# Performance work log

Hardware: AMD Instinct MI355X
Metric: run time of the kernel (lower is better)

Reference implementation:

```python
import jax, jax.numpy as jnp
import numpy as np
from jax import lax

IN_DIM, HID_DIM, OUT_DIM = 1024, 2048, 1024
N_EXP_A, TOPK_A, N_EXP_G = 12, 4, 6
BATCH = 2048
# Shannon entropy (nats) of {1/2, 1/3, 1/6}
H_TARGET = float(-(0.5 * np.log(0.5) + (1.0 / 3.0) * np.log(1.0 / 3.0) + (1.0 / 6.0) * np.log(1.0 / 6.0)))


def setup_inputs() -> dict:
    key = jax.random.key(0)
    ks = jax.random.split(key, 24)
    s_in = 1.0 / np.sqrt(IN_DIM)
    s_hid = 1.0 / np.sqrt(HID_DIM)
    s_out = 1.0 / np.sqrt(OUT_DIM)
    d = {}
    d['x'] = jax.random.normal(ks[0], (BATCH, IN_DIM), dtype=jnp.float32)
    # EngineA: gate + 12 experts (stacked)
    d['gate_a_w'] = jax.random.normal(ks[1], (IN_DIM, N_EXP_A), jnp.float32) * s_in
    d['gate_a_b'] = jnp.zeros((N_EXP_A,), jnp.float32)
    d['wa1'] = jax.random.normal(ks[2], (N_EXP_A, IN_DIM, HID_DIM), jnp.float32) * s_in
    d['ba1'] = jnp.zeros((N_EXP_A, HID_DIM), jnp.float32)
    d['wa2'] = jax.random.normal(ks[3], (N_EXP_A, HID_DIM, OUT_DIM), jnp.float32) * s_hid
    d['ba2'] = jnp.zeros((N_EXP_A, OUT_DIM), jnp.float32)
    # EngineG: gate + 6 experts (stacked)
    d['gate_g_w'] = jax.random.normal(ks[4], (IN_DIM, N_EXP_G), jnp.float32) * s_in
    d['gate_g_b'] = jnp.zeros((N_EXP_G,), jnp.float32)
    d['wg1'] = jax.random.normal(ks[5], (N_EXP_G, IN_DIM, HID_DIM), jnp.float32) * s_in
    d['bg1'] = jnp.zeros((N_EXP_G, HID_DIM), jnp.float32)
    d['wg2'] = jax.random.normal(ks[6], (N_EXP_G, HID_DIM, OUT_DIM), jnp.float32) * s_hid
    d['bg2'] = jnp.zeros((N_EXP_G, OUT_DIM), jnp.float32)
    # self_model: Linear(3,hid) Tanh Linear(hid,out) Tanh
    d['sm_w1'] = jax.random.normal(ks[7], (3, HID_DIM), jnp.float32) * (1.0 / np.sqrt(3.0))
    d['sm_b1'] = jnp.zeros((HID_DIM,), jnp.float32)
    d['sm_w2'] = jax.random.normal(ks[8], (HID_DIM, OUT_DIM), jnp.float32) * s_hid
    d['sm_b2'] = jnp.zeros((OUT_DIM,), jnp.float32)
    # self_influence Linear(out,out)
    d['si_w'] = jax.random.normal(ks[9], (OUT_DIM, OUT_DIM), jnp.float32) * s_out
    d['si_b'] = jnp.zeros((OUT_DIM,), jnp.float32)
    # field_transform Linear(out,out) + Tanh
    d['ft_w'] = jax.random.normal(ks[10], (OUT_DIM, OUT_DIM), jnp.float32) * s_out
    d['ft_b'] = jnp.zeros((OUT_DIM,), jnp.float32)
    d['tension_scale'] = jnp.asarray(1.0 / 3.0, jnp.float32)
    d['n_steps'] = 3
    return d


def _experts(x, w1, b1, w2, b2):
    # x:[B,I], w1:[E,I,H] -> [B,E,O]  (Linear-ReLU-Linear per expert)
    h = jax.nn.relu(jnp.einsum('bi,eih->beh', x, w1) + b1[None])
    return jnp.einsum('beh,eho->beo', h, w2) + b2[None]


def reference(x, gate_a_w, gate_a_b, wa1, ba1, wa2, ba2,
              gate_g_w, gate_g_b, wg1, bg1, wg2, bg2,
              sm_w1, sm_b1, sm_w2, sm_b2, si_w, si_b, ft_w, ft_b,
              tension_scale, n_steps):
    B = x.shape[0]
    # ---- EngineA: top-k (k=4 of 12) MoE ----
    logits_a = x @ gate_a_w + gate_a_b
    topv, topi = lax.top_k(logits_a, TOPK_A)
    topw = jax.nn.softmax(topv, axis=-1)
    weights_a = jnp.zeros_like(logits_a).at[jnp.arange(B)[:, None], topi].set(topw)
    out_a = _experts(x, wa1, ba1, wa2, ba2)            # [B,12,O]
    out_plus = jnp.einsum('be,beo->bo', weights_a, out_a)
    # ---- EngineG: dense-softmax MoE + entropy loss ----
    weights_g = jax.nn.softmax(x @ gate_g_w + gate_g_b, axis=-1)
    out_g = _experts(x, wg1, bg1, wg2, bg2)            # [B,6,O]
    out_minus = jnp.einsum('be,beo->bo', weights_g, out_g)
    h_ent = -(weights_g * jnp.log(weights_g + 1e-8)).sum(-1).mean()
    entropy_loss = (h_ent - H_TARGET) ** 2
    # ---- self-referential loop ----
    repulsion = out_plus - out_minus
    prev_tension = (repulsion ** 2).sum(-1, keepdims=True)      # [B,1]
    tensions = [lax.stop_gradient(prev_tension.mean())]          # .item() detaches
    modified_repulsion = repulsion
    for step in range(n_steps):
        tension_scalar = prev_tension.mean(-1, keepdims=True)    # [B,1]
        if step == 0:
            tension_delta = jnp.zeros_like(tension_scalar)
        else:
            tension_delta = tension_scalar - tensions[-1]
        step_tensor = jnp.full_like(tension_scalar, step / n_steps)
        self_input = jnp.concatenate([tension_scalar, tension_delta, step_tensor], -1)  # [B,3]
        self_state = jnp.tanh(jnp.tanh(self_input @ sm_w1 + sm_b1) @ sm_w2 + sm_b2)
        influence = self_state @ si_w + si_b
        modified_repulsion = repulsion + influence
        prev_tension = (modified_repulsion ** 2).sum(-1, keepdims=True)
        tensions.append(lax.stop_gradient(prev_tension.mean()))
    equilibrium = (out_plus + out_minus) * 0.5
    field_direction = jnp.tanh(modified_repulsion @ ft_w + ft_b)
    output = equilibrium + tension_scale * jnp.sqrt(prev_tension + 1e-8) * field_direction
    t = jnp.stack(tensions)
    convergence_loss = jnp.abs(t[1:] - t[:-1]).mean()            # built from .item()s -> constant
    aux_loss = entropy_loss + 0.001 * convergence_loss
    return output, aux_loss
```

## Files before the change

kernel.cpp:

```cpp
#include <hip/hip_runtime.h>

typedef _Float16 f16;
typedef f16  f16x8 __attribute__((ext_vector_type(8)));
typedef f16  f16x4 __attribute__((ext_vector_type(4)));
typedef float f32x4 __attribute__((ext_vector_type(4)));

#define LOAD_LDS16(gp, lp) __builtin_amdgcn_global_load_lds( \
    (const __attribute__((address_space(1))) void*)(gp),     \
    (__attribute__((address_space(3))) void*)(lp), 16, 0, 0)


__global__ __launch_bounds__(256) void castx_kernel(const float* __restrict__ x,
                                                    f16* __restrict__ o) {
  long i = ((long)blockIdx.x * 256 + threadIdx.x) * 4;
  const float4 v = *(const float4*)(x + i);
  f16x4 h; h.x = (f16)v.x; h.y = (f16)v.y; h.z = (f16)v.z; h.w = (f16)v.w;
  *(f16x4*)(o + i) = h;
}

__global__ __launch_bounds__(256) void transpose_cast(const float* __restrict__ src,
                                                      f16* __restrict__ dst,
                                                      int R, int C, long sbatch,
                                                      long dbatch, int dld) {
  __shared__ float tile[32][33];
  const int zc = blockIdx.x * 32;
  const int zr = blockIdx.y * 32;
  const int z  = blockIdx.z;
  const float* s = src + (long)z * sbatch;
  f16* d = dst + (long)z * dbatch;
  const int tx = threadIdx.x & 31, ty = threadIdx.x >> 5;
#pragma unroll
  for (int rr = 0; rr < 32; rr += 8)
    tile[ty + rr][tx] = s[(long)(zr + ty + rr) * C + (zc + tx)];
  __syncthreads();
#pragma unroll
  for (int rr = 0; rr < 32; rr += 8)
    d[(long)(zc + ty + rr) * dld + (zr + tx)] = (f16)tile[tx][ty + rr];
}

__global__ __launch_bounds__(256) void gating_kernel(
    const float* __restrict__ x, const float* __restrict__ gaw,
    const float* __restrict__ gab, const float* __restrict__ ggw,
    const float* __restrict__ ggb,
    float* __restrict__ wG, float* __restrict__ ent,
    int* __restrict__ rows, float* __restrict__ gval, int* __restrict__ cnt,
    int* __restrict__ eA, int* __restrict__ posA, float* __restrict__ wA4) {
  const int b = blockIdx.x, t = threadIdx.x;
  const float* xr = x + (long)b * 1024;
  float pa[12], pg[6];
#pragma unroll
  for (int e = 0; e < 12; e++) pa[e] = 0.f;
#pragma unroll
  for (int e = 0; e < 6; e++) pg[e] = 0.f;
  const int i0 = t * 4;
  const float4 xv = *(const float4*)(xr + i0);
  const float xs[4] = {xv.x, xv.y, xv.z, xv.w};
#pragma unroll
  for (int u = 0; u < 4; u++) {
    const float xi = xs[u];
    const float* ga = gaw + (long)(i0 + u) * 12;
    const float* gg = ggw + (long)(i0 + u) * 6;
#pragma unroll
    for (int e = 0; e < 12; e++) pa[e] += xi * ga[e];
#pragma unroll
    for (int e = 0; e < 6; e++) pg[e] += xi * gg[e];
  }
#pragma unroll
  for (int e = 0; e < 12; e++)
    for (int m = 1; m < 64; m <<= 1) pa[e] += __shfl_xor(pa[e], m);
#pragma unroll
  for (int e = 0; e < 6; e++)
    for (int m = 1; m < 64; m <<= 1) pg[e] += __shfl_xor(pg[e], m);
  __shared__ float rw[4][18];
  const int lane = t & 63, wv = t >> 6;
  if (lane == 0) {
#pragma unroll
    for (int e = 0; e < 12; e++) rw[wv][e] = pa[e];
#pragma unroll
    for (int e = 0; e < 6; e++) rw[wv][12 + e] = pg[e];
  }
  __syncthreads();
  if (t == 0) {
    float la[12], lg[6];
#pragma unroll
    for (int e = 0; e < 12; e++)
      la[e] = rw[0][e] + rw[1][e] + rw[2][e] + rw[3][e] + gab[e];
#pragma unroll
    for (int e = 0; e < 6; e++)
      lg[e] = rw[0][12 + e] + rw[1][12 + e] + rw[2][12 + e] + rw[3][12 + e] + ggb[e];
    unsigned used = 0; float tv[4]; int tix[4];
    for (int k = 0; k < 4; k++) {
      float best = -3.4e38f; int bi = 0;
      for (int e = 0; e < 12; e++)
        if (!((used >> e) & 1u) && la[e] > best) { best = la[e]; bi = e; }
      tv[k] = best; tix[k] = bi; used |= 1u << bi;
    }
    const float mx = tv[0];
    float s = 0.f, w4[4];
    for (int k = 0; k < 4; k++) { w4[k] = expf(tv[k] - mx); s += w4[k]; }
    for (int k = 0; k < 4; k++) {
      const float w = w4[k] / s;
      const int e = tix[k];
      const int pos = atomicAdd(&cnt[e], 1);
      rows[e * 2048 + pos] = b;
      gval[e * 2048 + pos] = w;
      eA[b * 4 + k] = e;
      posA[b * 4 + k] = pos;
      wA4[b * 4 + k] = w;
    }
    float mg = lg[0];
    for (int e = 1; e < 6; e++) mg = fmaxf(mg, lg[e]);
    float sg = 0.f, wg6[6];
    for (int e = 0; e < 6; e++) { wg6[e] = expf(lg[e] - mg); sg += wg6[e]; }
    float H = 0.f;
    for (int e = 0; e < 6; e++) {
      const float w = wg6[e] / sg;
      wG[b * 6 + e] = w;
      H -= w * logf(w + 1e-8f);
    }
    ent[b] = H;
  }
}

__global__ void base_kernel(const int* __restrict__ cnt, int* __restrict__ baseA) {
  if (threadIdx.x == 0 && blockIdx.x == 0) {
    int r = 0;
    for (int e = 0; e < 12; e++) { baseA[e] = r; r += cnt[e]; }
  }
}

__global__ __launch_bounds__(256) void combine_kernel(
    const f16* __restrict__ res, const int* __restrict__ eA,
    const int* __restrict__ posA, const float* __restrict__ wA4,
    const float* __restrict__ wG, const int* __restrict__ baseA,
    const float* __restrict__ ba2, const float* __restrict__ bg2,
    float* __restrict__ outP, float* __restrict__ outM,
    float* __restrict__ pt0, float* __restrict__ ts0) {
  const long b = blockIdx.x;
  const int t = threadIdx.x;
  const int c = t * 4;
  float4 P = {0.f, 0.f, 0.f, 0.f}, M = {0.f, 0.f, 0.f, 0.f};
#pragma unroll
  for (int k = 0; k < 4; k++) {
    const int e = eA[b * 4 + k];
    const long slot = baseA[e] + posA[b * 4 + k];
    const f16x4 v = *(const f16x4*)(res + slot * 1024 + c);
    const float w = wA4[b * 4 + k];
    const float4 bb = *(const float4*)(ba2 + (long)e * 1024 + c);
    P.x += (float)v.x + w * bb.x; P.y += (float)v.y + w * bb.y;
    P.z += (float)v.z + w * bb.z; P.w += (float)v.w + w * bb.w;
  }
#pragma unroll
  for (int e = 0; e < 6; e++) {
    const f16x4 v = *(const f16x4*)(res + (8192L + e * 2048 + b) * 1024 + c);
    const float w = wG[b * 6 + e];
    const float4 bb = *(const float4*)(bg2 + (long)e * 1024 + c);
    M.x += (float)v.x + w * bb.x; M.y += (float)v.y + w * bb.y;
    M.z += (float)v.z + w * bb.z; M.w += (float)v.w + w * bb.w;
  }
  *(float4*)(outP + b * 1024 + c) = P;
  *(float4*)(outM + b * 1024 + c) = M;
  const float dx = P.x - M.x, dy = P.y - M.y, dz = P.z - M.z, dw = P.w - M.w;
  float s = dx * dx + dy * dy + dz * dz + dw * dw;
#pragma unroll
  for (int m = 1; m < 64; m <<= 1) s += __shfl_xor(s, m);
  __shared__ float rw[4];
  if ((t & 63) == 0) rw[t >> 6] = s;
  __syncthreads();
  if (t == 0) {
    const float tot = rw[0] + rw[1] + rw[2] + rw[3];
    pt0[b] = tot;
    atomicAdd(ts0, tot);
  }
}

__global__ __launch_bounds__(256) void hsm_kernel(
    const float* __restrict__ pt, const float* __restrict__ tsum,
    const float* __restrict__ w1, const float* __restrict__ b1,
    f16* __restrict__ o, int step) {
  const int j = blockIdx.x * 256 + threadIdx.x;
  const int b0 = blockIdx.y * 64;
  const float u0 = w1[j], u1 = w1[2048 + j], u2 = w1[4096 + j], bb = b1[j];
  const float tm = tsum[0] * (1.f / 2048.f);
  const float st = (float)step * (1.f / 3.f);
#pragma unroll 4
  for (int r = 0; r < 64; r++) {
    const int b = b0 + r;
    const float t = pt[b];
    const float delta = (step == 0) ? 0.f : (t - tm);
    o[(long)b * 2048 + j] = (f16)tanhf(t * u0 + delta * u1 + st * u2 + bb);
  }
}

__global__ __launch_bounds__(256) void aux_kernel(const float* __restrict__ ent,
                                                  const float* __restrict__ tsum,
                                                  float* __restrict__ out) {
  const int t = threadIdx.x;
  float s = 0.f;
  for (int i = t; i < 2048; i += 256) s += ent[i];
#pragma unroll
  for (int m = 1; m < 64; m <<= 1) s += __shfl_xor(s, m);
  __shared__ float rw[4];
  if ((t & 63) == 0) rw[t >> 6] = s;
  __syncthreads();
  if (t == 0) {
    const float h = (rw[0] + rw[1] + rw[2] + rw[3]) * (1.f / 2048.f);
    const float d = h - 1.0114042647f;
    const float el = d * d;
    const float t0 = tsum[0] * (1.f / 2048.f), t1 = tsum[1] * (1.f / 2048.f);
    const float t2 = tsum[2] * (1.f / 2048.f), t3 = tsum[3] * (1.f / 2048.f);
    const float conv = (fabsf(t1 - t0) + fabsf(t2 - t1) + fabsf(t3 - t2)) * (1.f / 3.f);
    out[0] = el + 0.001f * conv;
  }
}

__global__ __launch_bounds__(256) void gemm1_kernel(
    const f16* __restrict__ x, const f16* __restrict__ w1t,
    const float* __restrict__ ba1, const float* __restrict__ bg1,
    f16* __restrict__ h, const int* __restrict__ rows,
    const float* __restrict__ gval, const int* __restrict__ cnt,
    const int* __restrict__ baseA, const float* __restrict__ wG) {
  __shared__ f16 Al[2][128 * 32];
  __shared__ f16 Bl[2][128 * 32];
  __shared__ int   Lrow[128];
  __shared__ float Lg[128];
  int id = blockIdx.x;
  int e18, mi, ni, live; long row0; const float* bp;
  if (id < 3072) {
    const int k = id & 7, t = id >> 3;
    mi = t & 15; const int pid = k * 24 + (t >> 4);
    const int e = pid >> 4; ni = pid & 15;
    live = cnt[e] - mi * 128;
    if (live <= 0) return;
    if (live > 128) live = 128;
    row0 = baseA[e] + mi * 128; e18 = e; bp = ba1 + (long)e * 2048;
  } else {
    id -= 3072;
    const int k = id & 7, t = id >> 3;
    mi = t & 15; const int pid = k * 12 + (t >> 4);
    const int e = pid >> 4; ni = pid & 15;
    row0 = 8192L + e * 2048 + mi * 128; live = 128;
    e18 = 12 + e; bp = bg1 + (long)e * 2048;
  }
  const int tid = threadIdx.x;
  const bool routed = (e18 < 12);
  if (tid < 128) {
    const int gi = mi * 128 + tid;
    if (routed) {
      const bool ok = tid < live;
      Lrow[tid] = ok ? rows[e18 * 2048 + gi] : 0;
      Lg[tid]   = ok ? gval[e18 * 2048 + gi] : 0.f;
    } else {
      Lrow[tid] = gi;
      Lg[tid] = wG[gi * 6 + (e18 - 12)];
    }
  }
  __syncthreads();
  const int r0 = Lrow[tid >> 2], r1 = Lrow[64 + (tid >> 2)];
  const f16* a0 = x + (long)r0 * 1024 + (tid & 3) * 8;
  const f16* a1 = x + (long)r1 * 1024 + (tid & 3) * 8;
  const f16* b0 = w1t + (long)e18 * 2048 * 1024 + ((long)ni * 128 + (tid >> 2)) * 1024 + (tid & 3) * 8;
  const f16* b1p = b0 + 64 * 1024;

  const int wave = tid >> 6, lane = tid & 63;
  const int wm = wave & 1, wn = wave >> 1;
  const int l16 = lane & 15, q = lane >> 4;
  f32x4 acc[4][4] = {};

  LOAD_LDS16(a0, &Al[0][tid * 8]);
  LOAD_LDS16(a1, &Al[0][(256 + tid) * 8]);
  LOAD_LDS16(b0, &Bl[0][tid * 8]);
  LOAD_LDS16(b1p, &Bl[0][(256 + tid) * 8]);
  for (int kk = 0; kk < 32; ++kk) {
    __syncthreads();
    const int cur = kk & 1;
    if (kk + 1 < 32) {
      const long k0 = (long)(kk + 1) * 32;
      const int nb = cur ^ 1;
      LOAD_LDS16(a0 + k0, &Al[nb][tid * 8]);
      LOAD_LDS16(a1 + k0, &Al[nb][(256 + tid) * 8]);
      LOAD_LDS16(b0 + k0, &Bl[nb][tid * 8]);
      LOAD_LDS16(b1p + k0, &Bl[nb][(256 + tid) * 8]);
    }
    f16x8 av[4], bv[4];
#pragma unroll
    for (int i = 0; i < 4; i++)
      av[i] = *(const f16x8*)&Al[cur][(wm * 64 + i * 16 + l16) * 32 + q * 8];
#pragma unroll
    for (int j = 0; j < 4; j++)
      bv[j] = *(const f16x8*)&Bl[cur][(wn * 64 + j * 16 + l16) * 32 + q * 8];
#pragma unroll
    for (int i = 0; i < 4; i++)
#pragma unroll
      for (int j = 0; j < 4; j++)
        acc[i][j] = __builtin_amdgcn_mfma_f32_16x16x32_f16(av[i], bv[j], acc[i][j], 0, 0, 0);
  }
#pragma unroll
  for (int i = 0; i < 4; i++) {
#pragma unroll
    for (int r = 0; r < 4; r++) {
      const int lr = wm * 64 + i * 16 + q * 4 + r;
      if (lr < live) {
        const float wv = Lg[lr];
        f16* C = h + (row0 + lr) * 2048;
#pragma unroll
        for (int j = 0; j < 4; j++) {
          const int gc = ni * 128 + wn * 64 + j * 16 + l16;
          const float v = fmaxf(acc[i][j][r] + bp[gc], 0.f) * wv;
          C[gc] = (f16)v;
        }
      }
    }
  }
}

__global__ __launch_bounds__(256) void gemm2_kernel(
    const f16* __restrict__ h, const f16* __restrict__ w2t,
    f16* __restrict__ res, const int* __restrict__ cnt,
    const int* __restrict__ baseA) {
  __shared__ f16 Al[2][128 * 32];
  __shared__ f16 Bl[2][64 * 32];
  int id = blockIdx.x;
  int e18, mi, ni, live; long row0;
  if (id < 3072) {
    const int k = id & 7, t = id >> 3;
    mi = t & 15; const int pid = k * 24 + (t >> 4);
    const int e = pid >> 4; ni = pid & 15;
    live = cnt[e] - mi * 128;
    if (live <= 0) return;
    if (live > 128) live = 128;
    row0 = baseA[e] + mi * 128; e18 = e;
  } else {
    id -= 3072;
    const int k = id & 7, t = id >> 3;
    mi = t & 15; const int pid = k * 12 + (t >> 4);
    const int e = pid >> 4; ni = pid & 15;
    row0 = 8192L + e * 2048 + mi * 128; live = 128; e18 = 12 + e;
  }
  const int tid = threadIdx.x;
  const f16* a0 = h + (row0 + (tid >> 2)) * 2048 + (tid & 3) * 8;
  const f16* a1 = a0 + 64 * 2048;
  const f16* b0 = w2t + (long)e18 * 1024 * 2048 + ((long)ni * 64 + (tid >> 2)) * 2048 + (tid & 3) * 8;

  const int wave = tid >> 6, lane = tid & 63;
  const int wm = wave & 1, wn = wave >> 1;
  const int l16 = lane & 15, q = lane >> 4;
  f32x4 acc[4][2] = {};

  LOAD_LDS16(a0, &Al[0][tid * 8]);
  LOAD_LDS16(a1, &Al[0][(256 + tid) * 8]);
  LOAD_LDS16(b0, &Bl[0][tid * 8]);
  for (int kk = 0; kk < 64; ++kk) {
    __syncthreads();
    const int cur = kk & 1;
    if (kk + 1 < 64) {
      const long k0 = (long)(kk + 1) * 32;
      const int nb = cur ^ 1;
      LOAD_LDS16(a0 + k0, &Al[nb][tid * 8]);
      LOAD_LDS16(a1 + k0, &Al[nb][(256 + tid) * 8]);
      LOAD_LDS16(b0 + k0, &Bl[nb][tid * 8]);
    }
    f16x8 av[4], bv[2];
#pragma unroll
    for (int i = 0; i < 4; i++)
      av[i] = *(const f16x8*)&Al[cur][(wm * 64 + i * 16 + l16) * 32 + q * 8];
#pragma unroll
    for (int j = 0; j < 2; j++)
      bv[j] = *(const f16x8*)&Bl[cur][(wn * 32 + j * 16 + l16) * 32 + q * 8];
#pragma unroll
    for (int i = 0; i < 4; i++)
#pragma unroll
      for (int j = 0; j < 2; j++)
        acc[i][j] = __builtin_amdgcn_mfma_f32_16x16x32_f16(av[i], bv[j], acc[i][j], 0, 0, 0);
  }
#pragma unroll
  for (int i = 0; i < 4; i++) {
#pragma unroll
    for (int r = 0; r < 4; r++) {
      const int lr = wm * 64 + i * 16 + q * 4 + r;
      if (lr < live) {
        f16* C = res + (row0 + lr) * 1024 + ni * 64;
#pragma unroll
        for (int j = 0; j < 2; j++) {
          const int gc = wn * 32 + j * 16 + l16;
          C[gc] = (f16)acc[i][j][r];
        }
      }
    }
  }
}


struct GA {
  const f16* A; long lda;
  const f16* B; long ldb;
  int nk;
  float* Cf; f16* Ch;
  const float* bias;
  const float* op; const float* om;
  const float* pt; const float* ts;
  float* pt_out; float* tsum_out;
};

template <int EPI>
__global__ __launch_bounds__(256) void gemm_s(GA a) {
  __shared__ f16 Al[2][64 * 32];
  __shared__ f16 Bl[2][64 * 32];
  const int tid = threadIdx.x;
  const int wave = tid >> 6, lane = tid & 63;
  const int wm = wave & 1, wn = wave >> 1;
  const int l16 = lane & 15, q = lane >> 4;
  const long m0 = (long)blockIdx.y * 64;
  const long n0 = (long)blockIdx.x * 64;
  const f16* a0 = a.A + (m0 + (tid >> 2)) * a.lda + (tid & 3) * 8;
  const f16* b0 = a.B + (n0 + (tid >> 2)) * a.ldb + (tid & 3) * 8;
  f32x4 acc[2][2] = {};
  LOAD_LDS16(a0, &Al[0][tid * 8]);
  LOAD_LDS16(b0, &Bl[0][tid * 8]);
  for (int kk = 0; kk < a.nk; ++kk) {
    __syncthreads();
    const int cur = kk & 1;
    if (kk + 1 < a.nk) {
      const long k0 = (long)(kk + 1) * 32;
      const int nb = cur ^ 1;
      LOAD_LDS16(a0 + k0, &Al[nb][tid * 8]);
      LOAD_LDS16(b0 + k0, &Bl[nb][tid * 8]);
    }
    f16x8 av[2], bv[2];
#pragma unroll
    for (int i = 0; i < 2; i++)
      av[i] = *(const f16x8*)&Al[cur][(wm * 32 + i * 16 + l16) * 32 + q * 8];
#pragma unroll
    for (int j = 0; j < 2; j++)
      bv[j] = *(const f16x8*)&Bl[cur][(wn * 32 + j * 16 + l16) * 32 + q * 8];
#pragma unroll
    for (int i = 0; i < 2; i++)
#pragma unroll
      for (int j = 0; j < 2; j++)
        acc[i][j] = __builtin_amdgcn_mfma_f32_16x16x32_f16(av[i], bv[j], acc[i][j], 0, 0, 0);
  }
  if constexpr (EPI == 2) {
#pragma unroll
    for (int i = 0; i < 2; i++)
#pragma unroll
      for (int r = 0; r < 4; r++) {
        const long gr = m0 + wm * 32 + i * 16 + q * 4 + r;
#pragma unroll
        for (int j = 0; j < 2; j++) {
          const int gc = (int)n0 + wn * 32 + j * 16 + l16;
          a.Ch[gr * 1024 + gc] = (f16)tanhf(acc[i][j][r] + a.bias[gc]);
        }
      }
  } else if constexpr (EPI == 3) {
    float wave_ss = 0.f;
#pragma unroll
    for (int i = 0; i < 2; i++)
#pragma unroll
      for (int r = 0; r < 4; r++) {
        const long gr = m0 + wm * 32 + i * 16 + q * 4 + r;
        float ss = 0.f;
#pragma unroll
        for (int j = 0; j < 2; j++) {
          const int gc = (int)n0 + wn * 32 + j * 16 + l16;
          const long ix = gr * 1024 + gc;
          const float v = (a.op[ix] - a.om[ix]) + acc[i][j][r] + a.bias[gc];
          a.Ch[ix] = (f16)v;
          ss += v * v;
        }
        ss += __shfl_xor(ss, 1); ss += __shfl_xor(ss, 2);
        ss += __shfl_xor(ss, 4); ss += __shfl_xor(ss, 8);
        if (l16 == 0) {
          atomicAdd(a.pt_out + gr, ss);
          wave_ss += ss;
        }
      }
    wave_ss += __shfl_xor(wave_ss, 16);
    wave_ss += __shfl_xor(wave_ss, 32);
    if (lane == 0) atomicAdd(a.tsum_out, wave_ss);
  } else {
    const float tsc = a.ts[0];
#pragma unroll
    for (int i = 0; i < 2; i++)
#pragma unroll
      for (int r = 0; r < 4; r++) {
        const long gr = m0 + wm * 32 + i * 16 + q * 4 + r;
        const float sq = sqrtf(a.pt[gr] + 1e-8f) * tsc;
#pragma unroll
        for (int j = 0; j < 2; j++) {
          const int gc = (int)n0 + wn * 32 + j * 16 + l16;
          const long ix = gr * 1024 + gc;
          const float v = tanhf(acc[i][j][r] + a.bias[gc]);
          a.Cf[ix] = 0.5f * (a.op[ix] + a.om[ix]) + sq * v;
        }
      }
  }
}


extern "C" void kernel_launch(void* const* d_in, const int* in_sizes, int n_in,
                              void* d_out, int out_size, void* d_ws, size_t ws_size,
                              hipStream_t stream) {
  (void)in_sizes; (void)n_in; (void)out_size; (void)ws_size;
  const float* x    = (const float*)d_in[0];
  const float* gaw  = (const float*)d_in[1];
  const float* gab  = (const float*)d_in[2];
  const float* wa1  = (const float*)d_in[3];
  const float* ba1  = (const float*)d_in[4];
  const float* wa2  = (const float*)d_in[5];
  const float* ba2  = (const float*)d_in[6];
  const float* ggw  = (const float*)d_in[7];
  const float* ggb  = (const float*)d_in[8];
  const float* wg1  = (const float*)d_in[9];
  const float* bg1  = (const float*)d_in[10];
  const float* wg2  = (const float*)d_in[11];
  const float* bg2  = (const float*)d_in[12];
  const float* smw1 = (const float*)d_in[13];
  const float* smb1 = (const float*)d_in[14];
  const float* smw2 = (const float*)d_in[15];
  const float* smb2 = (const float*)d_in[16];
  const float* siw  = (const float*)d_in[17];
  const float* sib  = (const float*)d_in[18];
  const float* ftw  = (const float*)d_in[19];
  const float* ftb  = (const float*)d_in[20];
  const float* tsc  = (const float*)d_in[21];

  char* p = (char*)d_ws;
  size_t off = 0;
  auto alloc = [&](size_t bytes) -> char* {
    char* r = p + off;
    off = (off + bytes + 255) & ~(size_t)255;
    return r;
  };
  f16* xb     = (f16*)alloc(2048UL * 1024 * 2);
  f16* w1t    = (f16*)alloc(18UL * 2048 * 1024 * 2);
  f16* smw2t  = (f16*)alloc(1024UL * 2048 * 2);
  f16* sit    = (f16*)alloc(1024UL * 1024 * 2);
  f16* ftt    = (f16*)alloc(1024UL * 1024 * 2);
  f16* h      = (f16*)alloc(20480UL * 2048 * 2);
  f16* res    = (f16*)alloc(20480UL * 1024 * 2);
  float* outP = (float*)alloc(2048UL * 1024 * 4);
  float* outM = (float*)alloc(2048UL * 1024 * 4);
  f16* hsmb   = (f16*)alloc(2048UL * 2048 * 2);
  f16* sst    = (f16*)alloc(2048UL * 1024 * 2);
  f16* modb   = (f16*)alloc(2048UL * 1024 * 2);
  float* entb = (float*)alloc(2048 * 4);
  float* wGb  = (float*)alloc(2048 * 6 * 4);
  float* ptb  = (float*)alloc(4 * 2048 * 4);
  float* tsb  = (float*)alloc(4 * 4);
  int*   cntb = (int*)alloc(12 * 4);
  int*   baseAb = (int*)alloc(12 * 4);
  int*   rowsb  = (int*)alloc(12 * 2048 * 4);
  float* gvalb  = (float*)alloc(12 * 2048 * 4);
  int*   eAb    = (int*)alloc(2048 * 4 * 4);
  int*   posAb  = (int*)alloc(2048 * 4 * 4);
  float* wA4b   = (float*)alloc(2048 * 4 * 4);

  f16* w2t = w1t;

  hipMemsetAsync(ptb, 0, 33072, stream);

  transpose_cast<<<dim3(64, 32, 12), 256, 0, stream>>>(wa1, w1t, 1024, 2048,
      1024L * 2048, 2048L * 1024, 1024);
  transpose_cast<<<dim3(64, 32, 6), 256, 0, stream>>>(wg1, w1t + 12UL * 2048 * 1024,
      1024, 2048, 1024L * 2048, 2048L * 1024, 1024);
  transpose_cast<<<dim3(32, 64, 1), 256, 0, stream>>>(smw2, smw2t, 2048, 1024, 0, 0, 2048);
  transpose_cast<<<dim3(32, 32, 1), 256, 0, stream>>>(siw, sit, 1024, 1024, 0, 0, 1024);
  transpose_cast<<<dim3(32, 32, 1), 256, 0, stream>>>(ftw, ftt, 1024, 1024, 0, 0, 1024);
  castx_kernel<<<2048, 256, 0, stream>>>(x, xb);
  gating_kernel<<<2048, 256, 0, stream>>>(x, gaw, gab, ggw, ggb, wGb, entb,
                                          rowsb, gvalb, cntb, eAb, posAb, wA4b);
  base_kernel<<<1, 64, 0, stream>>>(cntb, baseAb);

  gemm1_kernel<<<4608, 256, 0, stream>>>(xb, w1t, ba1, bg1, h,
                                         rowsb, gvalb, cntb, baseAb, wGb);

  transpose_cast<<<dim3(32, 64, 12), 256, 0, stream>>>(wa2, w2t, 2048, 1024,
      2048L * 1024, 1024L * 2048, 2048);
  transpose_cast<<<dim3(32, 64, 6), 256, 0, stream>>>(wg2, w2t + 12UL * 1024 * 2048,
      2048, 1024, 2048L * 1024, 1024L * 2048, 2048);

  gemm2_kernel<<<4608, 256, 0, stream>>>(h, w2t, res, cntb, baseAb);

  combine_kernel<<<2048, 256, 0, stream>>>(res, eAb, posAb, wA4b, wGb, baseAb,
                                           ba2, bg2, outP, outM, ptb, tsb);

  for (int s = 0; s < 3; s++) {
    hsm_kernel<<<dim3(8, 32), 256, 0, stream>>>(ptb + s * 2048, tsb + s, smw1, smb1, hsmb, s);
    GA g3{};
    g3.A = hsmb; g3.lda = 2048; g3.B = smw2t; g3.ldb = 2048; g3.nk = 64;
    g3.Ch = sst; g3.bias = smb2;
    gemm_s<2><<<dim3(16, 32), 256, 0, stream>>>(g3);
    GA g4{};
    g4.A = sst; g4.lda = 1024; g4.B = sit; g4.ldb = 1024; g4.nk = 32;
    g4.Ch = modb; g4.bias = sib; g4.op = outP; g4.om = outM;
    g4.pt_out = ptb + (s + 1) * 2048; g4.tsum_out = tsb + (s + 1);
    gemm_s<3><<<dim3(16, 32), 256, 0, stream>>>(g4);
  }

  GA g5{};
  g5.A = modb; g5.lda = 1024; g5.B = ftt; g5.ldb = 1024; g5.nk = 32;
  g5.Cf = (float*)d_out; g5.bias = ftb; g5.op = outP; g5.om = outM;
  g5.pt = ptb + 3 * 2048; g5.ts = tsc;
  gemm_s<4><<<dim3(16, 32), 256, 0, stream>>>(g5);

  aux_kernel<<<1, 256, 0, stream>>>(entb, tsb, (float*)d_out + 2048UL * 1024);
}
```

Baseline: 1.079 ms.

## Swizzle LDS tiles against bank conflicts and widen gemm2 N-tile to 128

```diff
diff --git a/kernel.cpp b/kernel.cpp
--- a/kernel.cpp
+++ b/kernel.cpp
@@ -256,15 +256,17 @@
     }
   }
   __syncthreads();
+  const int sc = ((tid & 3) ^ ((tid >> 3) & 3)) * 8;
   const int r0 = Lrow[tid >> 2], r1 = Lrow[64 + (tid >> 2)];
-  const f16* a0 = x + (long)r0 * 1024 + (tid & 3) * 8;
-  const f16* a1 = x + (long)r1 * 1024 + (tid & 3) * 8;
-  const f16* b0 = w1t + (long)e18 * 2048 * 1024 + ((long)ni * 128 + (tid >> 2)) * 1024 + (tid & 3) * 8;
+  const f16* a0 = x + (long)r0 * 1024 + sc;
+  const f16* a1 = x + (long)r1 * 1024 + sc;
+  const f16* b0 = w1t + (long)e18 * 2048 * 1024 + ((long)ni * 128 + (tid >> 2)) * 1024 + sc;
   const f16* b1p = b0 + 64 * 1024;
 
   const int wave = tid >> 6, lane = tid & 63;
   const int wm = wave & 1, wn = wave >> 1;
   const int l16 = lane & 15, q = lane >> 4;
+  const int qa = (q ^ ((l16 >> 1) & 3)) * 8;
   f32x4 acc[4][4] = {};
 
   LOAD_LDS16(a0, &Al[0][tid * 8]);
@@ -285,10 +287,10 @@
     f16x8 av[4], bv[4];
 #pragma unroll
     for (int i = 0; i < 4; i++)
-      av[i] = *(const f16x8*)&Al[cur][(wm * 64 + i * 16 + l16) * 32 + q * 8];
+      av[i] = *(const f16x8*)&Al[cur][(wm * 64 + i * 16 + l16) * 32 + qa];
 #pragma unroll
     for (int j = 0; j < 4; j++)
-      bv[j] = *(const f16x8*)&Bl[cur][(wn * 64 + j * 16 + l16) * 32 + q * 8];
+      bv[j] = *(const f16x8*)&Bl[cur][(wn * 64 + j * 16 + l16) * 32 + qa];
 #pragma unroll
     for (int i = 0; i < 4; i++)
 #pragma unroll
@@ -319,37 +321,41 @@
     f16* __restrict__ res, const int* __restrict__ cnt,
     const int* __restrict__ baseA) {
   __shared__ f16 Al[2][128 * 32];
-  __shared__ f16 Bl[2][64 * 32];
+  __shared__ f16 Bl[2][128 * 32];
   int id = blockIdx.x;
   int e18, mi, ni, live; long row0;
-  if (id < 3072) {
+  if (id < 1536) {
     const int k = id & 7, t = id >> 3;
-    mi = t & 15; const int pid = k * 24 + (t >> 4);
-    const int e = pid >> 4; ni = pid & 15;
+    mi = t & 15; const int pid = k * 12 + (t >> 4);
+    const int e = pid >> 3; ni = pid & 7;
     live = cnt[e] - mi * 128;
     if (live <= 0) return;
     if (live > 128) live = 128;
     row0 = baseA[e] + mi * 128; e18 = e;
   } else {
-    id -= 3072;
+    id -= 1536;
     const int k = id & 7, t = id >> 3;
-    mi = t & 15; const int pid = k * 12 + (t >> 4);
-    const int e = pid >> 4; ni = pid & 15;
+    mi = t & 15; const int pid = k * 6 + (t >> 4);
+    const int e = pid >> 3; ni = pid & 7;
     row0 = 8192L + e * 2048 + mi * 128; live = 128; e18 = 12 + e;
   }
   const int tid = threadIdx.x;
-  const f16* a0 = h + (row0 + (tid >> 2)) * 2048 + (tid & 3) * 8;
+  const int sc = ((tid & 3) ^ ((tid >> 3) & 3)) * 8;
+  const f16* a0 = h + (row0 + (tid >> 2)) * 2048 + sc;
   const f16* a1 = a0 + 64 * 2048;
-  const f16* b0 = w2t + (long)e18 * 1024 * 2048 + ((long)ni * 64 + (tid >> 2)) * 2048 + (tid & 3) * 8;
+  const f16* b0 = w2t + (long)e18 * 1024 * 2048 + ((long)ni * 128 + (tid >> 2)) * 2048 + sc;
+  const f16* b1p = b0 + 64 * 2048;
 
   const int wave = tid >> 6, lane = tid & 63;
   const int wm = wave & 1, wn = wave >> 1;
   const int l16 = lane & 15, q = lane >> 4;
-  f32x4 acc[4][2] = {};
+  const int qa = (q ^ ((l16 >> 1) & 3)) * 8;
+  f32x4 acc[4][4] = {};
 
   LOAD_LDS16(a0, &Al[0][tid * 8]);
   LOAD_LDS16(a1, &Al[0][(256 + tid) * 8]);
   LOAD_LDS16(b0, &Bl[0][tid * 8]);
+  LOAD_LDS16(b1p, &Bl[0][(256 + tid) * 8]);
   for (int kk = 0; kk < 64; ++kk) {
     __syncthreads();
     const int cur = kk & 1;
@@ -359,18 +365,19 @@
       LOAD_LDS16(a0 + k0, &Al[nb][tid * 8]);
       LOAD_LDS16(a1 + k0, &Al[nb][(256 + tid) * 8]);
       LOAD_LDS16(b0 + k0, &Bl[nb][tid * 8]);
-    }
-    f16x8 av[4], bv[2];
+      LOAD_LDS16(b1p + k0, &Bl[nb][(256 + tid) * 8]);
+    }
+    f16x8 av[4], bv[4];
 #pragma unroll
     for (int i = 0; i < 4; i++)
-      av[i] = *(const f16x8*)&Al[cur][(wm * 64 + i * 16 + l16) * 32 + q * 8];
-#pragma unroll
-    for (int j = 0; j < 2; j++)
-      bv[j] = *(const f16x8*)&Bl[cur][(wn * 32 + j * 16 + l16) * 32 + q * 8];
+      av[i] = *(const f16x8*)&Al[cur][(wm * 64 + i * 16 + l16) * 32 + qa];
+#pragma unroll
+    for (int j = 0; j < 4; j++)
+      bv[j] = *(const f16x8*)&Bl[cur][(wn * 64 + j * 16 + l16) * 32 + qa];
 #pragma unroll
     for (int i = 0; i < 4; i++)
 #pragma unroll
-      for (int j = 0; j < 2; j++)
+      for (int j = 0; j < 4; j++)
         acc[i][j] = __builtin_amdgcn_mfma_f32_16x16x32_f16(av[i], bv[j], acc[i][j], 0, 0, 0);
   }
 #pragma unroll
@@ -379,10 +386,10 @@
     for (int r = 0; r < 4; r++) {
       const int lr = wm * 64 + i * 16 + q * 4 + r;
       if (lr < live) {
-        f16* C = res + (row0 + lr) * 1024 + ni * 64;
-#pragma unroll
-        for (int j = 0; j < 2; j++) {
-          const int gc = wn * 32 + j * 16 + l16;
+        f16* C = res + (row0 + lr) * 1024 + ni * 128;
+#pragma unroll
+        for (int j = 0; j < 4; j++) {
+          const int gc = wn * 64 + j * 16 + l16;
           C[gc] = (f16)acc[i][j][r];
         }
       }
@@ -410,10 +417,12 @@
   const int wave = tid >> 6, lane = tid & 63;
   const int wm = wave & 1, wn = wave >> 1;
   const int l16 = lane & 15, q = lane >> 4;
+  const int qa = (q ^ ((l16 >> 1) & 3)) * 8;
   const long m0 = (long)blockIdx.y * 64;
   const long n0 = (long)blockIdx.x * 64;
-  const f16* a0 = a.A + (m0 + (tid >> 2)) * a.lda + (tid & 3) * 8;
-  const f16* b0 = a.B + (n0 + (tid >> 2)) * a.ldb + (tid & 3) * 8;
+  const int sc = ((tid & 3) ^ ((tid >> 3) & 3)) * 8;
+  const f16* a0 = a.A + (m0 + (tid >> 2)) * a.lda + sc;
+  const f16* b0 = a.B + (n0 + (tid >> 2)) * a.ldb + sc;
   f32x4 acc[2][2] = {};
   LOAD_LDS16(a0, &Al[0][tid * 8]);
   LOAD_LDS16(b0, &Bl[0][tid * 8]);
@@ -429,10 +438,10 @@
     f16x8 av[2], bv[2];
 #pragma unroll
     for (int i = 0; i < 2; i++)
-      av[i] = *(const f16x8*)&Al[cur][(wm * 32 + i * 16 + l16) * 32 + q * 8];
+      av[i] = *(const f16x8*)&Al[cur][(wm * 32 + i * 16 + l16) * 32 + qa];
 #pragma unroll
     for (int j = 0; j < 2; j++)
-      bv[j] = *(const f16x8*)&Bl[cur][(wn * 32 + j * 16 + l16) * 32 + q * 8];
+      bv[j] = *(const f16x8*)&Bl[cur][(wn * 32 + j * 16 + l16) * 32 + qa];
 #pragma unroll
     for (int i = 0; i < 2; i++)
 #pragma unroll
@@ -579,7 +588,7 @@
   transpose_cast<<<dim3(32, 64, 6), 256, 0, stream>>>(wg2, w2t + 12UL * 1024 * 2048,
       2048, 1024, 2048L * 1024, 1024L * 2048, 2048);
 
-  gemm2_kernel<<<4608, 256, 0, stream>>>(h, w2t, res, cntb, baseAb);
+  gemm2_kernel<<<2304, 256, 0, stream>>>(h, w2t, res, cntb, baseAb);
 
   combine_kernel<<<2048, 256, 0, stream>>>(res, eAb, posAb, wA4b, wGb, baseAb,
                                            ba2, bg2, outP, outM, ptb, tsb);
```

Result: faster. 1.042 ms (-3.4%).
